# Kernel optimization log

Hardware: AMD Instinct MI355X
Metric: run time of the kernel (lower is better)

## Reference

```python
import jax, jax.numpy as jnp
import numpy as np

D = 128   # edge_feature_size
E = 128   # number of edges in edge_feature_s_list
B = 4096  # true_batch_size


def setup_inputs() -> dict:
    key = jax.random.key(0)
    k1, k2, k3, k4 = jax.random.split(key, 4)
    temporal_edge_feature = jax.random.normal(k1, (B, D), dtype=jnp.float32)
    edge_feature_s = jax.random.normal(k2, (E, B, D), dtype=jnp.float32)
    W = jax.random.normal(k3, (D, D), dtype=jnp.float32) * (1.0 / np.sqrt(D))
    b = jax.random.normal(k4, (D,), dtype=jnp.float32) * 0.01
    return {
        "true_batch_size": B,
        "temporal_edge_feature": temporal_edge_feature,
        "edge_feature_s": edge_feature_s,
        "W": W,
        "b": b,
    }


def reference(true_batch_size, temporal_edge_feature, edge_feature_s, W, b):
    # Linear projection (same weights applied to source and each edge)
    m_i = temporal_edge_feature @ W.T + b            # [B, D]
    m_j = jnp.einsum('ebd,fd->ebf', edge_feature_s, W) + b  # [E, B, D]
    # Per-(edge, batch) dot-product score
    e_ij = jnp.einsum('bd,ebd->eb', m_i, m_j)        # [E, B]
    # Plain sum-normalization over edges (NOT softmax, faithful to source)
    e_j_sum = jnp.sum(e_ij, axis=0, keepdims=True)   # [1, B]
    weights = e_ij / e_j_sum                         # [E, B]
    # Weighted edge features
    out = weights[:, :, None] * edge_feature_s       # [E, B, D]
    return out
```

## Files before the change

kernel.cpp:

```cpp
#include <hip/hip_runtime.h>

constexpr int D    = 128;
constexpr int E    = 128;
constexpr int BB   = 4096;
constexpr int ROWS = 8;

typedef float f32x4 __attribute__((ext_vector_type(4)));


__global__ __launch_bounds__(128) void gwh_kernel(
    const float* __restrict__ W, const float* __restrict__ bias, float* out)
{
    __shared__ float Wl[D][D];
    __shared__ float bl[D];
    const int t = threadIdx.x;
    const int r = blockIdx.x;

    const float4* W4 = (const float4*)W;
    float4* Wl4 = (float4*)&Wl[0][0];
    for (int i = t; i < D * D / 4; i += 128) Wl4[i] = W4[i];
    bl[t] = bias[t];
    __syncthreads();

    float acc = 0.f;
    for (int k = 0; k < D; ++k) acc += Wl[k][r] * Wl[k][t];
    out[(size_t)2 * BB * D + r * D + t] = acc;

    if (r == 0) {
        float hh = 0.f;
        for (int f = 0; f < D; ++f) hh += bl[f] * Wl[f][t];
        out[(size_t)3 * BB * D + t] = hh;
        if (t == 0) {
            float b2 = 0.f;
            for (int f = 0; f < D; ++f) b2 += bl[f] * bl[f];
            out[(size_t)3 * BB * D + D] = b2;
        }
    }
}

__global__ __launch_bounds__(256) void prep2_kernel(
    const float* __restrict__ T, float* out)
{
    __shared__ float Gl[D][D];
    __shared__ float Tl[ROWS][D];
    __shared__ float hl[D];
    __shared__ float beta_s;

    const int t  = threadIdx.x;
    const int b0 = blockIdx.x * ROWS;

    {
        const float4* Gs = (const float4*)(out + (size_t)2 * BB * D);
        float4* Gd = (float4*)&Gl[0][0];
        for (int i = t; i < D * D / 4; i += 256) Gd[i] = Gs[i];
        const float4* Ts = (const float4*)(T + (size_t)b0 * D);
        ((float4*)&Tl[0][0])[t] = Ts[t];
        if (t < D) hl[t] = out[(size_t)3 * BB * D + t];
        if (t == 0) beta_s = out[(size_t)3 * BB * D + D];
    }
    __syncthreads();

    const int dc = t & 127;
    const int r0 = (t >> 7) * 4;
    float a0 = hl[dc], a1 = hl[dc], a2 = hl[dc], a3 = hl[dc];
    #pragma unroll 4
    for (int k = 0; k < D; k += 4) {
        const float g0 = Gl[k + 0][dc], g1 = Gl[k + 1][dc],
                    g2 = Gl[k + 2][dc], g3 = Gl[k + 3][dc];
        const float4 t0 = *(const float4*)&Tl[r0 + 0][k];
        const float4 t1 = *(const float4*)&Tl[r0 + 1][k];
        const float4 t2 = *(const float4*)&Tl[r0 + 2][k];
        const float4 t3 = *(const float4*)&Tl[r0 + 3][k];
        a0 += t0.x * g0 + t0.y * g1 + t0.z * g2 + t0.w * g3;
        a1 += t1.x * g0 + t1.y * g1 + t1.z * g2 + t1.w * g3;
        a2 += t2.x * g0 + t2.y * g1 + t2.z * g2 + t2.w * g3;
        a3 += t3.x * g0 + t3.y * g1 + t3.z * g2 + t3.w * g3;
    }
    out[(size_t)(b0 + r0 + 0) * D + dc] = a0;
    out[(size_t)(b0 + r0 + 1) * D + dc] = a1;
    out[(size_t)(b0 + r0 + 2) * D + dc] = a2;
    out[(size_t)(b0 + r0 + 3) * D + dc] = a3;

    const int cr = t >> 5, cl = t & 31;
    const float4 tc = *(const float4*)&Tl[cr][cl * 4];
    const float4 hc = *(const float4*)&hl[cl * 4];
    float p = tc.x * hc.x + tc.y * hc.y + tc.z * hc.z + tc.w * hc.w;
    #pragma unroll
    for (int msk = 16; msk >= 1; msk >>= 1) p += __shfl_xor(p, msk);
    if (cl == 0) out[(size_t)(BB + b0 + cr) * D] = p + beta_s;
}

__global__ __launch_bounds__(256) void att_main(
    const float* __restrict__ S, float* out)
{
    const int b  = blockIdx.x;
    const int t  = threadIdx.x;
    const int lc = t & 31;
    const int eb = t >> 5;

    __shared__ float sc[E];
    __shared__ float inv_s;

    const f32x4* Sp = (const f32x4*)S;
    const f32x4  v4 = ((const f32x4*)(out + (size_t)b * D))[lc];
    const float  c  = out[(size_t)(BB + b) * D];

    f32x4 s[16];
    #pragma unroll
    for (int i = 0; i < 16; ++i) {
        const int e = i * 8 + eb;
        s[i] = __builtin_nontemporal_load(Sp + ((size_t)e * BB + b) * 32 + lc);
    }

    #pragma unroll
    for (int i = 0; i < 16; ++i) {
        float p = s[i].x * v4.x + s[i].y * v4.y + s[i].z * v4.z + s[i].w * v4.w;
        #pragma unroll
        for (int msk = 16; msk >= 1; msk >>= 1) p += __shfl_xor(p, msk);
        if (lc == 0) sc[i * 8 + eb] = p + c;
    }
    __syncthreads();

    if (t < 64) {
        double d0 = (double)sc[t] + (double)sc[t + 64];
        #pragma unroll
        for (int msk = 32; msk >= 1; msk >>= 1) d0 += __shfl_xor(d0, msk);
        if (t == 0) inv_s = (float)(1.0 / d0);
    }
    __syncthreads();

    const float inv = inv_s;
    f32x4* Op = (f32x4*)out;
    #pragma unroll
    for (int i = 0; i < 16; ++i) {
        const int e = i * 8 + eb;
        const float w = sc[e] * inv;
        f32x4 o = s[i] * w;
        __builtin_nontemporal_store(o, Op + ((size_t)e * BB + b) * 32 + lc);
    }
}

extern "C" void kernel_launch(void* const* d_in, const int* in_sizes, int n_in,
                              void* d_out, int out_size, void* d_ws, size_t ws_size,
                              hipStream_t stream) {
    const float* T    = (const float*)d_in[1];
    const float* S    = (const float*)d_in[2];
    const float* W    = (const float*)d_in[3];
    const float* bias = (const float*)d_in[4];
    float* out        = (float*)d_out;

    gwh_kernel<<<D, D, 0, stream>>>(W, bias, out);
    prep2_kernel<<<BB / ROWS, 256, 0, stream>>>(T, out);
    att_main<<<BB, 256, 0, stream>>>(S, out);
}
```

Measured before the change: 467.3 us.

## Fuse per-row projection into attention kernel using workspace for Gram matrix

Moves the precomputed Gram matrix and bias terms into the workspace buffer and adds a fused kernel that computes each batch row's projected vector and constant inline before scoring edges. This drops the prep2 launch and its round trip through the output buffer. The cost is that every block now re-reads the 64KB Gram matrix from L2 with strided per-thread loads. The old three-kernel path is kept as a fallback when no workspace is provided.

```diff
diff --git a/kernel.cpp b/kernel.cpp
--- a/kernel.cpp
+++ b/kernel.cpp
@@ -9,7 +9,7 @@
 
 
 __global__ __launch_bounds__(128) void gwh_kernel(
-    const float* __restrict__ W, const float* __restrict__ bias, float* out)
+    const float* __restrict__ W, const float* __restrict__ bias, float* P)
 {
     __shared__ float Wl[D][D];
     __shared__ float bl[D];
@@ -24,22 +24,100 @@
 
     float acc = 0.f;
     for (int k = 0; k < D; ++k) acc += Wl[k][r] * Wl[k][t];
-    out[(size_t)2 * BB * D + r * D + t] = acc;
+    P[r * D + t] = acc;
 
     if (r == 0) {
         float hh = 0.f;
         for (int f = 0; f < D; ++f) hh += bl[f] * Wl[f][t];
-        out[(size_t)3 * BB * D + t] = hh;
+        P[D * D + t] = hh;
         if (t == 0) {
             float b2 = 0.f;
             for (int f = 0; f < D; ++f) b2 += bl[f] * bl[f];
-            out[(size_t)3 * BB * D + D] = b2;
+            P[D * D + D] = b2;
         }
     }
 }
 
+__global__ __launch_bounds__(256) void att_fused(
+    const float* __restrict__ S, const float* __restrict__ T,
+    const float* __restrict__ P, float* out)
+{
+    const int b  = blockIdx.x;
+    const int t  = threadIdx.x;
+    const int lc = t & 31;
+    const int eb = t >> 5;
+
+    __shared__ float vl[2][D];
+    __shared__ float sc[E];
+    __shared__ float inv_s, c_s;
+
+    const f32x4* Sp = (const f32x4*)S;
+
+    f32x4 s[16];
+    #pragma unroll
+    for (int i = 0; i < 16; ++i) {
+        const int e = i * 8 + eb;
+        s[i] = __builtin_nontemporal_load(Sp + ((size_t)e * BB + b) * 32 + lc);
+    }
+
+    {
+        const int d  = t & 127;
+        const int kh = (t >> 7) * 64;
+        const float* Trow = T + (size_t)b * D;
+        float acc = 0.f;
+        #pragma unroll 8
+        for (int kk = 0; kk < 64; ++kk)
+            acc += Trow[kh + kk] * P[(size_t)(kh + kk) * D + d];
+        vl[t >> 7][d] = acc;
+    }
+    if (t < 32) {
+        const f32x4 t4 = ((const f32x4*)(T + (size_t)b * D))[t];
+        const f32x4 h4 = ((const f32x4*)(P + D * D))[t];
+        float p = t4.x * h4.x + t4.y * h4.y + t4.z * h4.z + t4.w * h4.w;
+        #pragma unroll
+        for (int m = 16; m >= 1; m >>= 1) p += __shfl_xor(p, m);
+        if (t == 0) c_s = p + P[D * D + D];
+    }
+    __syncthreads();
+
+    f32x4 v4;
+    {
+        const f32x4 va = ((const f32x4*)&vl[0][0])[lc];
+        const f32x4 vb = ((const f32x4*)&vl[1][0])[lc];
+        const f32x4 h4 = ((const f32x4*)(P + D * D))[lc];
+        v4 = va + vb + h4;
+    }
+    const float c = c_s;
+
+    #pragma unroll
+    for (int i = 0; i < 16; ++i) {
+        float p = s[i].x * v4.x + s[i].y * v4.y + s[i].z * v4.z + s[i].w * v4.w;
+        #pragma unroll
+        for (int m = 16; m >= 1; m >>= 1) p += __shfl_xor(p, m);
+        if (lc == 0) sc[i * 8 + eb] = p + c;
+    }
+    __syncthreads();
+
+    if (t < 64) {
+        double d0 = (double)sc[t] + (double)sc[t + 64];
+        #pragma unroll
+        for (int m = 32; m >= 1; m >>= 1) d0 += __shfl_xor(d0, m);
+        if (t == 0) inv_s = (float)(1.0 / d0);
+    }
+    __syncthreads();
+
+    const float inv = inv_s;
+    f32x4* Op = (f32x4*)out;
+    #pragma unroll
+    for (int i = 0; i < 16; ++i) {
+        const int e = i * 8 + eb;
+        const float w = sc[e] * inv;
+        __builtin_nontemporal_store(s[i] * w, Op + ((size_t)e * BB + b) * 32 + lc);
+    }
+}
+
 __global__ __launch_bounds__(256) void prep2_kernel(
-    const float* __restrict__ T, float* out)
+    const float* __restrict__ T, const float* __restrict__ P, float* out)
 {
     __shared__ float Gl[D][D];
     __shared__ float Tl[ROWS][D];
@@ -50,13 +128,13 @@
     const int b0 = blockIdx.x * ROWS;
 
     {
-        const float4* Gs = (const float4*)(out + (size_t)2 * BB * D);
+        const float4* Gs = (const float4*)P;
         float4* Gd = (float4*)&Gl[0][0];
         for (int i = t; i < D * D / 4; i += 256) Gd[i] = Gs[i];
         const float4* Ts = (const float4*)(T + (size_t)b0 * D);
         ((float4*)&Tl[0][0])[t] = Ts[t];
-        if (t < D) hl[t] = out[(size_t)3 * BB * D + t];
-        if (t == 0) beta_s = out[(size_t)3 * BB * D + D];
+        if (t < D) hl[t] = P[D * D + t];
+        if (t == 0) beta_s = P[D * D + D];
     }
     __syncthreads();
 
@@ -135,8 +213,7 @@
     for (int i = 0; i < 16; ++i) {
         const int e = i * 8 + eb;
         const float w = sc[e] * inv;
-        f32x4 o = s[i] * w;
-        __builtin_nontemporal_store(o, Op + ((size_t)e * BB + b) * 32 + lc);
+        __builtin_nontemporal_store(s[i] * w, Op + ((size_t)e * BB + b) * 32 + lc);
     }
 }
 
@@ -149,7 +226,15 @@
     const float* bias = (const float*)d_in[4];
     float* out        = (float*)d_out;
 
-    gwh_kernel<<<D, D, 0, stream>>>(W, bias, out);
-    prep2_kernel<<<BB / ROWS, 256, 0, stream>>>(T, out);
-    att_main<<<BB, 256, 0, stream>>>(S, out);
-}
+    const size_t need = (size_t)(D * D + D + 1) * sizeof(float);
+    if (d_ws != nullptr && ws_size >= need) {
+        float* P = (float*)d_ws;
+        gwh_kernel<<<D, D, 0, stream>>>(W, bias, P);
+        att_fused<<<BB, 256, 0, stream>>>(S, T, P, out);
+    } else {
+        float* P = out + (size_t)2 * BB * D;
+        gwh_kernel<<<D, D, 0, stream>>>(W, bias, P);
+        prep2_kernel<<<BB / ROWS, 256, 0, stream>>>(T, P, out);
+        att_main<<<BB, 256, 0, stream>>>(S, out);
+    }
+}
```

New measurement: 465.7 us. Within noise of the previous version (-0.3%).
